# Kernel optimization log

Measured on AMD Instinct MI355X. Metric: run time of the kernel, lower is better.

The kernel has to match this reference:

```python
import jax, jax.numpy as jnp
import numpy as np

B, S, D = 2, 2048, 1024
H, DH = 16, 64  # num_heads, hidden_dimension (per-head)


def setup_inputs() -> dict:
    key = jax.random.key(0)
    ks = jax.random.split(key, 9)
    s = 1.0 / np.sqrt(D)
    so = 1.0 / np.sqrt(H * DH)
    return {
        "x": jax.random.normal(ks[0], (B, S, D), dtype=jnp.float32),
        "Wq": jax.random.uniform(ks[1], (D, H * DH), jnp.float32, -s, s),
        "bq": jax.random.uniform(ks[2], (H * DH,), jnp.float32, -s, s),
        "Wk": jax.random.uniform(ks[3], (D, H * DH), jnp.float32, -s, s),
        "bk": jax.random.uniform(ks[4], (H * DH,), jnp.float32, -s, s),
        "Wv": jax.random.uniform(ks[5], (D, H * DH), jnp.float32, -s, s),
        "bv": jax.random.uniform(ks[6], (H * DH,), jnp.float32, -s, s),
        "Wo": jax.random.uniform(ks[7], (H * DH, D), jnp.float32, -so, so),
        "bo": jax.random.uniform(ks[8], (D,), jnp.float32, -so, so),
    }


def reference(x, Wq, bq, Wk, bk, Wv, bv, Wo, bo):
    b, s, _ = x.shape
    # project and split heads: [b, h, s, dh]
    q = (x @ Wq + bq).reshape(b, s, H, DH).transpose(0, 2, 1, 3)
    k = (x @ Wk + bk).reshape(b, s, H, DH).transpose(0, 2, 1, 3)
    v = (x @ Wv + bv).reshape(b, s, H, DH).transpose(0, 2, 1, 3)
    scores = jnp.einsum('bhqd,bhkd->bhqk', q, k) / jnp.sqrt(jnp.float32(DH))
    causal = jnp.triu(jnp.ones((s, s), dtype=bool), k=1)
    scores = jnp.where(causal, -jnp.inf, scores)
    weights = jax.nn.softmax(scores, axis=-1)
    out = jnp.einsum('bhqk,bhkd->bhqd', weights, v)
    out = out.transpose(0, 2, 1, 3).reshape(b, s, H * DH)
    return out @ Wo + bo
```

## Files before the change

kernel.cpp:

```cpp
#include <hip/hip_runtime.h>

#define B_  2
#define S_  2048
#define D_  1024
#define H_  16
#define DH_ 64
#define NDH (H_*DH_)
#define BS_ (B_*S_)
#define PER ((size_t)B_*H_*S_*DH_)

typedef __bf16 bf16;
typedef bf16 bf16x8 __attribute__((ext_vector_type(8)));
typedef bf16 bf16x4 __attribute__((ext_vector_type(4)));
typedef float f32x4 __attribute__((ext_vector_type(4)));

#define AS1 __attribute__((address_space(1)))
#define AS3 __attribute__((address_space(3)))
__device__ inline void gld16(const bf16* g, bf16* l) {
    __builtin_amdgcn_global_load_lds((const AS1 void*)g, (AS3 void*)l, 16, 0, 0);
}

__global__ __launch_bounds__(256) void prep(
        const float* __restrict__ x,
        const float* __restrict__ W0, const float* __restrict__ W1,
        const float* __restrict__ W2, const float* __restrict__ W3,
        bf16* __restrict__ xb, bf16* __restrict__ T0, bf16* __restrict__ T1,
        bf16* __restrict__ T2, bf16* __restrict__ T3) {
    __shared__ float T[32][33];
    int bid = blockIdx.x, t = threadIdx.x;
    if (bid < 4096) {
        int i = (bid * 256 + t) * 4;
        float4 v = *(const float4*)(x + i);
        bf16x4 o = { (bf16)v.x, (bf16)v.y, (bf16)v.z, (bf16)v.w };
        *(bf16x4*)(xb + i) = o;
        return;
    }
    int r2 = bid - 4096;
    int z = r2 >> 10, w = r2 & 1023;
    const float* W = (z == 0) ? W0 : (z == 1) ? W1 : (z == 2) ? W2 : W3;
    bf16* Wt = (z == 0) ? T0 : (z == 1) ? T1 : (z == 2) ? T2 : T3;
    int k0 = (w >> 5) * 32, n0 = (w & 31) * 32;
    int r = t >> 3, c = (t & 7) * 4;
    float4 v = *(const float4*)(W + (size_t)(k0 + r) * 1024 + n0 + c);
    T[c + 0][r] = v.x; T[c + 1][r] = v.y; T[c + 2][r] = v.z; T[c + 3][r] = v.w;
    __syncthreads();
    bf16x4 o = { (bf16)T[r][c], (bf16)T[r][c + 1], (bf16)T[r][c + 2], (bf16)T[r][c + 3] };
    *(bf16x4*)(Wt + (size_t)(n0 + r) * 1024 + k0 + c) = o;
}

__global__ __launch_bounds__(256) void qkv_gemm(
        const bf16* __restrict__ A, const bf16* __restrict__ Bt,
        const float* __restrict__ bq, const float* __restrict__ bk,
        const float* __restrict__ bv, bf16* __restrict__ Qout, bf16* __restrict__ Vt) {
    __shared__ __align__(16) bf16 As[128 * 32];
    __shared__ __align__(16) bf16 Bs[128 * 32];
    int tid = threadIdx.x, wave = tid >> 6, lane = tid & 63;
    int quad = lane >> 4, l16 = lane & 15;
    int bm = blockIdx.y * 128, bn = blockIdx.x * 128;
    int wm = (wave >> 1) * 64, wn = (wave & 1) * 64;

    int sr = lane >> 2, sc = (lane & 3) * 8;
    const bf16* Ag0 = A + (size_t)(bm + (wave * 2 + 0) * 16 + sr) * 1024 + sc;
    const bf16* Ag1 = A + (size_t)(bm + (wave * 2 + 1) * 16 + sr) * 1024 + sc;
    const bf16* Bg0 = Bt + (size_t)(bn + (wave * 2 + 0) * 16 + sr) * 1024 + sc;
    const bf16* Bg1 = Bt + (size_t)(bn + (wave * 2 + 1) * 16 + sr) * 1024 + sc;
    bf16* Al0 = &As[(wave * 2 + 0) * 512];
    bf16* Al1 = &As[(wave * 2 + 1) * 512];
    bf16* Bl0 = &Bs[(wave * 2 + 0) * 512];
    bf16* Bl1 = &Bs[(wave * 2 + 1) * 512];

    f32x4 acc[4][4] = {};

    for (int k0 = 0; k0 < 1024; k0 += 32) {
        gld16(Ag0 + k0, Al0);
        gld16(Ag1 + k0, Al1);
        gld16(Bg0 + k0, Bl0);
        gld16(Bg1 + k0, Bl1);
        __syncthreads();
        bf16x8 af[4], bfr[4];
        #pragma unroll
        for (int i = 0; i < 4; ++i)
            af[i] = *(const bf16x8*)&As[(wm + i * 16 + l16) * 32 + quad * 8];
        #pragma unroll
        for (int j = 0; j < 4; ++j)
            bfr[j] = *(const bf16x8*)&Bs[(wn + j * 16 + l16) * 32 + quad * 8];
        #pragma unroll
        for (int i = 0; i < 4; ++i)
          #pragma unroll
          for (int j = 0; j < 4; ++j)
            acc[i][j] = __builtin_amdgcn_mfma_f32_16x16x32_bf16(af[i], bfr[j], acc[i][j], 0, 0, 0);
        __syncthreads();
    }

    #pragma unroll
    for (int i = 0; i < 4; ++i)
      #pragma unroll
      for (int j = 0; j < 4; ++j) {
        int col = bn + wn + j * 16 + l16;
        float bias = (col < 1024) ? bq[col] : (col < 2048) ? bk[col - 1024] : bv[col - 2048];
        int qkv = col >> 10, cw = col & 1023;
        int hh = cw >> 6, d = cw & 63;
        int row0 = bm + wm + i * 16 + quad * 4;
        int bb = row0 >> 11, s0 = row0 & 2047;
        if (qkv < 2) {
            #pragma unroll
            for (int r = 0; r < 4; ++r)
                Qout[(size_t)qkv * PER + (((size_t)bb * H_ + hh) * S_ + s0 + r) * DH_ + d] =
                    (bf16)(acc[i][j][r] + bias);
        } else {
            bf16x4 pack;
            #pragma unroll
            for (int r = 0; r < 4; ++r) pack[r] = (bf16)(acc[i][j][r] + bias);
            *(bf16x4*)&Vt[(((size_t)bb * H_ + hh) * DH_ + d) * S_ + s0] = pack;
        }
      }
}

__global__ __launch_bounds__(256) void gemm128f(
        const bf16* __restrict__ A, const bf16* __restrict__ Bt,
        const float* __restrict__ bias, float* __restrict__ out) {
    __shared__ __align__(16) bf16 As[128 * 32];
    __shared__ __align__(16) bf16 Bs[128 * 32];
    int tid = threadIdx.x, wave = tid >> 6, lane = tid & 63;
    int quad = lane >> 4, l16 = lane & 15;
    int bm = blockIdx.y * 128, bn = blockIdx.x * 128;
    int wm = (wave >> 1) * 64, wn = (wave & 1) * 64;

    int sr = lane >> 2, sc = (lane & 3) * 8;
    const bf16* Ag0 = A + (size_t)(bm + (wave * 2 + 0) * 16 + sr) * 1024 + sc;
    const bf16* Ag1 = A + (size_t)(bm + (wave * 2 + 1) * 16 + sr) * 1024 + sc;
    const bf16* Bg0 = Bt + (size_t)(bn + (wave * 2 + 0) * 16 + sr) * 1024 + sc;
    const bf16* Bg1 = Bt + (size_t)(bn + (wave * 2 + 1) * 16 + sr) * 1024 + sc;
    bf16* Al0 = &As[(wave * 2 + 0) * 512];
    bf16* Al1 = &As[(wave * 2 + 1) * 512];
    bf16* Bl0 = &Bs[(wave * 2 + 0) * 512];
    bf16* Bl1 = &Bs[(wave * 2 + 1) * 512];

    f32x4 acc[4][4] = {};

    for (int k0 = 0; k0 < 1024; k0 += 32) {
        gld16(Ag0 + k0, Al0);
        gld16(Ag1 + k0, Al1);
        gld16(Bg0 + k0, Bl0);
        gld16(Bg1 + k0, Bl1);
        __syncthreads();
        bf16x8 af[4], bfr[4];
        #pragma unroll
        for (int i = 0; i < 4; ++i)
            af[i] = *(const bf16x8*)&As[(wm + i * 16 + l16) * 32 + quad * 8];
        #pragma unroll
        for (int j = 0; j < 4; ++j)
            bfr[j] = *(const bf16x8*)&Bs[(wn + j * 16 + l16) * 32 + quad * 8];
        #pragma unroll
        for (int i = 0; i < 4; ++i)
          #pragma unroll
          for (int j = 0; j < 4; ++j)
            acc[i][j] = __builtin_amdgcn_mfma_f32_16x16x32_bf16(af[i], bfr[j], acc[i][j], 0, 0, 0);
        __syncthreads();
    }

    #pragma unroll
    for (int i = 0; i < 4; ++i)
      #pragma unroll
      for (int j = 0; j < 4; ++j) {
        int col = bn + wn + j * 16 + l16;
        float b = bias[col];
        #pragma unroll
        for (int r = 0; r < 4; ++r) {
            int row = bm + wm + i * 16 + quad * 4 + r;
            out[(size_t)row * 1024 + col] = acc[i][j][r] + b;
        }
      }
}

__global__ __launch_bounds__(256) void flash4(
        const bf16* __restrict__ Q, const bf16* __restrict__ K,
        const bf16* __restrict__ Vt, bf16* __restrict__ O) {
    int bh = blockIdx.x;
    int b = bh >> 4, h = bh & 15;
    int pr = blockIdx.y;
    int tid = threadIdx.x;
    int wave = tid >> 6, lane = tid & 63;
    int quad = lane >> 4, l16 = lane & 15;

    __shared__ __align__(16) char smem[4 * 2 * 16 * 72 * 2];
    bf16 (*P)[2][16][72] = reinterpret_cast<bf16 (*)[2][16][72]>(smem);
    float (*redO)[4][64][4] = reinterpret_cast<float (*)[4][64][4]>(smem);
    __shared__ float redL[4][2][4][4];

    const bf16* Qb = Q + (size_t)bh * S_ * DH_;
    const bf16* Kb = K + (size_t)bh * S_ * DH_;
    const bf16* Vb = Vt + (size_t)bh * DH_ * S_;

    bf16x8 ones;
    #pragma unroll
    for (int j = 0; j < 8; ++j) ones[j] = (l16 == 0) ? (bf16)1.0f : (bf16)0.0f;

    for (int half = 0; half < 2; ++half) {
        int tile = half ? (63 - pr) : pr;
        int q0 = tile * 32;

        bf16x8 qf[2][2];
        #pragma unroll
        for (int s = 0; s < 2; ++s) {
            const bf16* qp = Qb + (size_t)(q0 + s * 16 + l16) * DH_ + quad * 8;
            qf[s][0] = *(const bf16x8*)(qp);
            qf[s][1] = *(const bf16x8*)(qp + 32);
        }

        f32x4 oacc[2][4] = {};
        f32x4 lacc[2] = {};

        int nkt = tile / 2 + 1;
        for (int kt = wave; kt < nkt; kt += 4) {
            int kv0 = kt * 64;
            bf16x8 kf[4][2];
            #pragma unroll
            for (int ns = 0; ns < 4; ++ns) {
                const bf16* kp = Kb + (size_t)(kv0 + ns * 16 + l16) * DH_ + quad * 8;
                kf[ns][0] = *(const bf16x8*)(kp);
                kf[ns][1] = *(const bf16x8*)(kp + 32);
            }
            f32x4 sacc[2][4] = {};
            #pragma unroll
            for (int s = 0; s < 2; ++s)
              #pragma unroll
              for (int ns = 0; ns < 4; ++ns) {
                sacc[s][ns] = __builtin_amdgcn_mfma_f32_16x16x32_bf16(qf[s][0], kf[ns][0], sacc[s][ns], 0, 0, 0);
                sacc[s][ns] = __builtin_amdgcn_mfma_f32_16x16x32_bf16(qf[s][1], kf[ns][1], sacc[s][ns], 0, 0, 0);
              }
            bool diag = (kt == nkt - 1);
            #pragma unroll
            for (int s = 0; s < 2; ++s)
              #pragma unroll
              for (int ns = 0; ns < 4; ++ns)
                #pragma unroll
                for (int r = 0; r < 4; ++r) {
                    float p = __expf(sacc[s][ns][r] * 0.125f);
                    if (diag) {
                        int kv = kv0 + ns * 16 + l16;
                        int qq = q0 + s * 16 + quad * 4 + r;
                        if (kv > qq) p = 0.f;
                    }
                    P[wave][s][quad * 4 + r][ns * 16 + l16] = (bf16)p;
                }
            #pragma unroll
            for (int ks = 0; ks < 2; ++ks) {
                bf16x8 pf0 = *(const bf16x8*)&P[wave][0][l16][ks * 32 + quad * 8];
                bf16x8 pf1 = *(const bf16x8*)&P[wave][1][l16][ks * 32 + quad * 8];
                lacc[0] = __builtin_amdgcn_mfma_f32_16x16x32_bf16(pf0, ones, lacc[0], 0, 0, 0);
                lacc[1] = __builtin_amdgcn_mfma_f32_16x16x32_bf16(pf1, ones, lacc[1], 0, 0, 0);
                #pragma unroll
                for (int ds = 0; ds < 4; ++ds) {
                    bf16x8 vf = *(const bf16x8*)(Vb + (size_t)(ds * 16 + l16) * S_ + kv0 + ks * 32 + quad * 8);
                    oacc[0][ds] = __builtin_amdgcn_mfma_f32_16x16x32_bf16(pf0, vf, oacc[0][ds], 0, 0, 0);
                    oacc[1][ds] = __builtin_amdgcn_mfma_f32_16x16x32_bf16(pf1, vf, oacc[1][ds], 0, 0, 0);
                }
            }
        }

        if (l16 == 0) {
            #pragma unroll
            for (int s = 0; s < 2; ++s)
              #pragma unroll
              for (int r = 0; r < 4; ++r)
                redL[wave][s][quad][r] = lacc[s][r];
        }
        #pragma unroll
        for (int s = 0; s < 2; ++s) {
            __syncthreads();
            #pragma unroll
            for (int ds = 0; ds < 4; ++ds)
                *(f32x4*)&redO[wave][ds][lane][0] = oacc[s][ds];
            __syncthreads();
            f32x4 osum = {};
            #pragma unroll
            for (int w = 0; w < 4; ++w)
                osum += *(const f32x4*)&redO[w][wave][lane][0];
            #pragma unroll
            for (int r = 0; r < 4; ++r) {
                float lsum = redL[0][s][quad][r] + redL[1][s][quad][r]
                           + redL[2][s][quad][r] + redL[3][s][quad][r];
                int qq = q0 + s * 16 + quad * 4 + r;
                O[((size_t)b * S_ + qq) * NDH + h * DH_ + wave * 16 + l16] = (bf16)(osum[r] / lsum);
            }
        }
        __syncthreads();
    }
}

extern "C" void kernel_launch(void* const* d_in, const int* in_sizes, int n_in,
                              void* d_out, int out_size, void* d_ws, size_t ws_size,
                              hipStream_t stream) {
    const float* x  = (const float*)d_in[0];
    const float* Wq = (const float*)d_in[1];
    const float* bq = (const float*)d_in[2];
    const float* Wk = (const float*)d_in[3];
    const float* bk = (const float*)d_in[4];
    const float* Wv = (const float*)d_in[5];
    const float* bv = (const float*)d_in[6];
    const float* Wo = (const float*)d_in[7];
    const float* bo = (const float*)d_in[8];
    float* out = (float*)d_out;

    bf16* ws = (bf16*)d_ws;
    const size_t M1 = (size_t)1024 * 1024;
    bf16* xb    = ws;
    bf16* WqkvT = ws + 4 * M1;
    bf16* WoT   = ws + 7 * M1;
    bf16* Qw    = ws + 8 * M1;
    bf16* Vtw   = ws + 16 * M1;
    bf16* Ow    = ws + 20 * M1;

    prep<<<8192, 256, 0, stream>>>(x, Wq, Wk, Wv, Wo,
                                   xb, WqkvT, WqkvT + M1, WqkvT + 2 * M1, WoT);

    qkv_gemm<<<dim3(3072 / 128, BS_ / 128), 256, 0, stream>>>(xb, WqkvT, bq, bk, bv, Qw, Vtw);

    flash4<<<dim3(B_ * H_, 32), 256, 0, stream>>>(Qw, Qw + PER, Vtw, Ow);

    gemm128f<<<dim3(1024 / 128, BS_ / 128), 256, 0, stream>>>(Ow, WoT, bo, out);
}
```

Baseline: 219.5 us.

## Software-pipeline PV step with double-buffered P and fold softmax scale into Q

Folds the 1/sqrt(64)*log2(e) factor into Q at the QKV GEMM epilogue so the attention kernel can use a raw exp2 instead of a scaled __expf. The flash kernel double-buffers the per-wave P tile in shared memory and defers each tile's PV matmul to the next iteration, so it overlaps with the following QK^T and exp work. It also pads P rows to 76 to change LDS bank mapping and adds a launch-bounds occupancy hint. The cost is twice the LDS for P and extra live registers from the pipelining, which could limit occupancy.

```diff
diff --git a/kernel.cpp b/kernel.cpp
--- a/kernel.cpp
+++ b/kernel.cpp
@@ -19,6 +19,14 @@
 __device__ inline void gld16(const bf16* g, bf16* l) {
     __builtin_amdgcn_global_load_lds((const AS1 void*)g, (AS3 void*)l, 16, 0, 0);
 }
+
+#if __has_builtin(__builtin_amdgcn_exp2f)
+#define EXP2(x) __builtin_amdgcn_exp2f(x)
+#else
+#define EXP2(x) exp2f(x)
+#endif
+
+#define QSCALE 0.18033688011112042f
 
 __global__ __launch_bounds__(256) void prep(
         const float* __restrict__ x,
@@ -102,10 +110,15 @@
         int hh = cw >> 6, d = cw & 63;
         int row0 = bm + wm + i * 16 + quad * 4;
         int bb = row0 >> 11, s0 = row0 & 2047;
-        if (qkv < 2) {
+        if (qkv == 0) {
             #pragma unroll
             for (int r = 0; r < 4; ++r)
-                Qout[(size_t)qkv * PER + (((size_t)bb * H_ + hh) * S_ + s0 + r) * DH_ + d] =
+                Qout[(((size_t)bb * H_ + hh) * S_ + s0 + r) * DH_ + d] =
+                    (bf16)((acc[i][j][r] + bias) * QSCALE);
+        } else if (qkv == 1) {
+            #pragma unroll
+            for (int r = 0; r < 4; ++r)
+                Qout[PER + (((size_t)bb * H_ + hh) * S_ + s0 + r) * DH_ + d] =
                     (bf16)(acc[i][j][r] + bias);
         } else {
             bf16x4 pack;
@@ -173,7 +186,8 @@
       }
 }
 
-__global__ __launch_bounds__(256) void flash4(
+#define PPAD 76
+__global__ __launch_bounds__(256, 4) void flash5(
         const bf16* __restrict__ Q, const bf16* __restrict__ K,
         const bf16* __restrict__ Vt, bf16* __restrict__ O) {
     int bh = blockIdx.x;
@@ -183,8 +197,8 @@
     int wave = tid >> 6, lane = tid & 63;
     int quad = lane >> 4, l16 = lane & 15;
 
-    __shared__ __align__(16) char smem[4 * 2 * 16 * 72 * 2];
-    bf16 (*P)[2][16][72] = reinterpret_cast<bf16 (*)[2][16][72]>(smem);
+    __shared__ __align__(16) char smem[2 * 4 * 2 * 16 * PPAD * 2];
+    bf16 (*P)[4][2][16][PPAD] = reinterpret_cast<bf16 (*)[4][2][16][PPAD]>(smem);
     float (*redO)[4][64][4] = reinterpret_cast<float (*)[4][64][4]>(smem);
     __shared__ float redL[4][2][4][4];
 
@@ -211,7 +225,24 @@
         f32x4 oacc[2][4] = {};
         f32x4 lacc[2] = {};
 
+        auto pv_step = [&](int pb, int kv0p) {
+            #pragma unroll
+            for (int ks = 0; ks < 2; ++ks) {
+                bf16x8 pf0 = *(const bf16x8*)&P[pb][wave][0][l16][ks * 32 + quad * 8];
+                bf16x8 pf1 = *(const bf16x8*)&P[pb][wave][1][l16][ks * 32 + quad * 8];
+                lacc[0] = __builtin_amdgcn_mfma_f32_16x16x32_bf16(pf0, ones, lacc[0], 0, 0, 0);
+                lacc[1] = __builtin_amdgcn_mfma_f32_16x16x32_bf16(pf1, ones, lacc[1], 0, 0, 0);
+                #pragma unroll
+                for (int ds = 0; ds < 4; ++ds) {
+                    bf16x8 vf = *(const bf16x8*)(Vb + (size_t)(ds * 16 + l16) * S_ + kv0p + ks * 32 + quad * 8);
+                    oacc[0][ds] = __builtin_amdgcn_mfma_f32_16x16x32_bf16(pf0, vf, oacc[0][ds], 0, 0, 0);
+                    oacc[1][ds] = __builtin_amdgcn_mfma_f32_16x16x32_bf16(pf1, vf, oacc[1][ds], 0, 0, 0);
+                }
+            }
+        };
+
         int nkt = tile / 2 + 1;
+        int buf = 0, kvp = -1;
         for (int kt = wave; kt < nkt; kt += 4) {
             int kv0 = kt * 64;
             bf16x8 kf[4][2];
@@ -221,43 +252,33 @@
                 kf[ns][0] = *(const bf16x8*)(kp);
                 kf[ns][1] = *(const bf16x8*)(kp + 32);
             }
-            f32x4 sacc[2][4] = {};
-            #pragma unroll
-            for (int s = 0; s < 2; ++s)
-              #pragma unroll
-              for (int ns = 0; ns < 4; ++ns) {
-                sacc[s][ns] = __builtin_amdgcn_mfma_f32_16x16x32_bf16(qf[s][0], kf[ns][0], sacc[s][ns], 0, 0, 0);
-                sacc[s][ns] = __builtin_amdgcn_mfma_f32_16x16x32_bf16(qf[s][1], kf[ns][1], sacc[s][ns], 0, 0, 0);
-              }
+            if (kvp >= 0) pv_step(buf ^ 1, kvp);
             bool diag = (kt == nkt - 1);
             #pragma unroll
-            for (int s = 0; s < 2; ++s)
-              #pragma unroll
-              for (int ns = 0; ns < 4; ++ns)
+            for (int s = 0; s < 2; ++s) {
+                f32x4 sacc[4] = {};
                 #pragma unroll
-                for (int r = 0; r < 4; ++r) {
-                    float p = __expf(sacc[s][ns][r] * 0.125f);
+                for (int ns = 0; ns < 4; ++ns) {
+                    sacc[ns] = __builtin_amdgcn_mfma_f32_16x16x32_bf16(qf[s][0], kf[ns][0], sacc[ns], 0, 0, 0);
+                    sacc[ns] = __builtin_amdgcn_mfma_f32_16x16x32_bf16(qf[s][1], kf[ns][1], sacc[ns], 0, 0, 0);
+                }
+                #pragma unroll
+                for (int ns = 0; ns < 4; ++ns)
+                  #pragma unroll
+                  for (int r = 0; r < 4; ++r) {
+                    float p = EXP2(sacc[ns][r]);
                     if (diag) {
                         int kv = kv0 + ns * 16 + l16;
                         int qq = q0 + s * 16 + quad * 4 + r;
                         if (kv > qq) p = 0.f;
                     }
-                    P[wave][s][quad * 4 + r][ns * 16 + l16] = (bf16)p;
-                }
-            #pragma unroll
-            for (int ks = 0; ks < 2; ++ks) {
-                bf16x8 pf0 = *(const bf16x8*)&P[wave][0][l16][ks * 32 + quad * 8];
-                bf16x8 pf1 = *(const bf16x8*)&P[wave][1][l16][ks * 32 + quad * 8];
-                lacc[0] = __builtin_amdgcn_mfma_f32_16x16x32_bf16(pf0, ones, lacc[0], 0, 0, 0);
-                lacc[1] = __builtin_amdgcn_mfma_f32_16x16x32_bf16(pf1, ones, lacc[1], 0, 0, 0);
-                #pragma unroll
-                for (int ds = 0; ds < 4; ++ds) {
-                    bf16x8 vf = *(const bf16x8*)(Vb + (size_t)(ds * 16 + l16) * S_ + kv0 + ks * 32 + quad * 8);
-                    oacc[0][ds] = __builtin_amdgcn_mfma_f32_16x16x32_bf16(pf0, vf, oacc[0][ds], 0, 0, 0);
-                    oacc[1][ds] = __builtin_amdgcn_mfma_f32_16x16x32_bf16(pf1, vf, oacc[1][ds], 0, 0, 0);
-                }
+                    P[buf][wave][s][quad * 4 + r][ns * 16 + l16] = (bf16)p;
+                  }
             }
-        }
+            kvp = kv0;
+            buf ^= 1;
+        }
+        if (kvp >= 0) pv_step(buf ^ 1, kvp);
 
         if (l16 == 0) {
             #pragma unroll
@@ -317,7 +338,7 @@
 
     qkv_gemm<<<dim3(3072 / 128, BS_ / 128), 256, 0, stream>>>(xb, WqkvT, bq, bk, bv, Qw, Vtw);
 
-    flash4<<<dim3(B_ * H_, 32), 256, 0, stream>>>(Qw, Qw + PER, Vtw, Ow);
+    flash5<<<dim3(B_ * H_, 32), 256, 0, stream>>>(Qw, Qw + PER, Vtw, Ow);
 
     gemm128f<<<dim3(1024 / 128, BS_ / 128), 256, 0, stream>>>(Ow, WoT, bo, out);
 }
```

Result: slower. 288.7 us (+31.5%).

## Prefetch next K tile in flash kernel and fold softmax scale into Q

Applied to the files above, without the earlier changes.

The QKV GEMM epilogue now multiplies Q by 0.125*log2(e), so the attention kernel can use exp2 directly on the scores instead of a scale followed by __expf. The flash kernel loads the K fragments for the next tile in two halves, one before and one after the P·V MFMAs, so global loads overlap with compute. P and the reduction buffer now get separate shared-memory arrays, and the P row pitch is padded from 72 to 76 to change the LDS bank pattern. The prefetch raises register pressure and the extra shared memory may lower occupancy; as before, softmax has no max subtraction, and Q is now rounded to bf16 after scaling.

```diff
diff --git a/kernel.cpp b/kernel.cpp
--- a/kernel.cpp
+++ b/kernel.cpp
@@ -19,6 +19,8 @@
 __device__ inline void gld16(const bf16* g, bf16* l) {
     __builtin_amdgcn_global_load_lds((const AS1 void*)g, (AS3 void*)l, 16, 0, 0);
 }
+
+#define QSCALE 0.18033688011112042f
 
 __global__ __launch_bounds__(256) void prep(
         const float* __restrict__ x,
@@ -102,10 +104,15 @@
         int hh = cw >> 6, d = cw & 63;
         int row0 = bm + wm + i * 16 + quad * 4;
         int bb = row0 >> 11, s0 = row0 & 2047;
-        if (qkv < 2) {
+        if (qkv == 0) {
             #pragma unroll
             for (int r = 0; r < 4; ++r)
-                Qout[(size_t)qkv * PER + (((size_t)bb * H_ + hh) * S_ + s0 + r) * DH_ + d] =
+                Qout[(((size_t)bb * H_ + hh) * S_ + s0 + r) * DH_ + d] =
+                    (bf16)((acc[i][j][r] + bias) * QSCALE);
+        } else if (qkv == 1) {
+            #pragma unroll
+            for (int r = 0; r < 4; ++r)
+                Qout[PER + (((size_t)bb * H_ + hh) * S_ + s0 + r) * DH_ + d] =
                     (bf16)(acc[i][j][r] + bias);
         } else {
             bf16x4 pack;
@@ -173,7 +180,8 @@
       }
 }
 
-__global__ __launch_bounds__(256) void flash4(
+#define PPAD 76
+__global__ __launch_bounds__(256) void flash7(
         const bf16* __restrict__ Q, const bf16* __restrict__ K,
         const bf16* __restrict__ Vt, bf16* __restrict__ O) {
     int bh = blockIdx.x;
@@ -183,9 +191,8 @@
     int wave = tid >> 6, lane = tid & 63;
     int quad = lane >> 4, l16 = lane & 15;
 
-    __shared__ __align__(16) char smem[4 * 2 * 16 * 72 * 2];
-    bf16 (*P)[2][16][72] = reinterpret_cast<bf16 (*)[2][16][72]>(smem);
-    float (*redO)[4][64][4] = reinterpret_cast<float (*)[4][64][4]>(smem);
+    __shared__ __align__(16) float redO[4][4][64][4];
+    __shared__ __align__(16) bf16 Pm[4][2][16][PPAD];
     __shared__ float redL[4][2][4][4];
 
     const bf16* Qb = Q + (size_t)bh * S_ * DH_;
@@ -212,23 +219,40 @@
         f32x4 lacc[2] = {};
 
         int nkt = tile / 2 + 1;
+
+        bf16x8 kfa[4][2];
+        {
+            int kt0 = (wave < nkt) ? wave : 0;
+            #pragma unroll
+            for (int ns = 0; ns < 4; ++ns) {
+                const bf16* kp = Kb + (size_t)(kt0 * 64 + ns * 16 + l16) * DH_ + quad * 8;
+                kfa[ns][0] = *(const bf16x8*)(kp);
+                kfa[ns][1] = *(const bf16x8*)(kp + 32);
+            }
+        }
+
         for (int kt = wave; kt < nkt; kt += 4) {
             int kv0 = kt * 64;
-            bf16x8 kf[4][2];
-            #pragma unroll
-            for (int ns = 0; ns < 4; ++ns) {
-                const bf16* kp = Kb + (size_t)(kv0 + ns * 16 + l16) * DH_ + quad * 8;
-                kf[ns][0] = *(const bf16x8*)(kp);
-                kf[ns][1] = *(const bf16x8*)(kp + 32);
-            }
+            int ktn = (kt + 4 < nkt) ? kt + 4 : kt;
+            int kvn = ktn * 64;
+
             f32x4 sacc[2][4] = {};
             #pragma unroll
             for (int s = 0; s < 2; ++s)
               #pragma unroll
               for (int ns = 0; ns < 4; ++ns) {
-                sacc[s][ns] = __builtin_amdgcn_mfma_f32_16x16x32_bf16(qf[s][0], kf[ns][0], sacc[s][ns], 0, 0, 0);
-                sacc[s][ns] = __builtin_amdgcn_mfma_f32_16x16x32_bf16(qf[s][1], kf[ns][1], sacc[s][ns], 0, 0, 0);
+                sacc[s][ns] = __builtin_amdgcn_mfma_f32_16x16x32_bf16(qf[s][0], kfa[ns][0], sacc[s][ns], 0, 0, 0);
+                sacc[s][ns] = __builtin_amdgcn_mfma_f32_16x16x32_bf16(qf[s][1], kfa[ns][1], sacc[s][ns], 0, 0, 0);
               }
+
+            bf16x8 kfb[2][2];
+            #pragma unroll
+            for (int ns = 0; ns < 2; ++ns) {
+                const bf16* kp = Kb + (size_t)(kvn + ns * 16 + l16) * DH_ + quad * 8;
+                kfb[ns][0] = *(const bf16x8*)(kp);
+                kfb[ns][1] = *(const bf16x8*)(kp + 32);
+            }
+
             bool diag = (kt == nkt - 1);
             #pragma unroll
             for (int s = 0; s < 2; ++s)
@@ -236,18 +260,19 @@
               for (int ns = 0; ns < 4; ++ns)
                 #pragma unroll
                 for (int r = 0; r < 4; ++r) {
-                    float p = __expf(sacc[s][ns][r] * 0.125f);
+                    float p = __builtin_exp2f(sacc[s][ns][r]);
                     if (diag) {
                         int kv = kv0 + ns * 16 + l16;
                         int qq = q0 + s * 16 + quad * 4 + r;
                         if (kv > qq) p = 0.f;
                     }
-                    P[wave][s][quad * 4 + r][ns * 16 + l16] = (bf16)p;
+                    Pm[wave][s][quad * 4 + r][ns * 16 + l16] = (bf16)p;
                 }
+
             #pragma unroll
             for (int ks = 0; ks < 2; ++ks) {
-                bf16x8 pf0 = *(const bf16x8*)&P[wave][0][l16][ks * 32 + quad * 8];
-                bf16x8 pf1 = *(const bf16x8*)&P[wave][1][l16][ks * 32 + quad * 8];
+                bf16x8 pf0 = *(const bf16x8*)&Pm[wave][0][l16][ks * 32 + quad * 8];
+                bf16x8 pf1 = *(const bf16x8*)&Pm[wave][1][l16][ks * 32 + quad * 8];
                 lacc[0] = __builtin_amdgcn_mfma_f32_16x16x32_bf16(pf0, ones, lacc[0], 0, 0, 0);
                 lacc[1] = __builtin_amdgcn_mfma_f32_16x16x32_bf16(pf1, ones, lacc[1], 0, 0, 0);
                 #pragma unroll
@@ -256,6 +281,15 @@
                     oacc[0][ds] = __builtin_amdgcn_mfma_f32_16x16x32_bf16(pf0, vf, oacc[0][ds], 0, 0, 0);
                     oacc[1][ds] = __builtin_amdgcn_mfma_f32_16x16x32_bf16(pf1, vf, oacc[1][ds], 0, 0, 0);
                 }
+            }
+
+            kfa[0][0] = kfb[0][0]; kfa[0][1] = kfb[0][1];
+            kfa[1][0] = kfb[1][0]; kfa[1][1] = kfb[1][1];
+            #pragma unroll
+            for (int ns = 2; ns < 4; ++ns) {
+                const bf16* kp = Kb + (size_t)(kvn + ns * 16 + l16) * DH_ + quad * 8;
+                kfa[ns][0] = *(const bf16x8*)(kp);
+                kfa[ns][1] = *(const bf16x8*)(kp + 32);
             }
         }
 
@@ -317,7 +351,7 @@
 
     qkv_gemm<<<dim3(3072 / 128, BS_ / 128), 256, 0, stream>>>(xb, WqkvT, bq, bk, bv, Qw, Vtw);
 
-    flash4<<<dim3(B_ * H_, 32), 256, 0, stream>>>(Qw, Qw + PER, Vtw, Ow);
+    flash7<<<dim3(B_ * H_, 32), 256, 0, stream>>>(Qw, Qw + PER, Vtw, Ow);
 
     gemm128f<<<dim3(1024 / 128, BS_ / 128), 256, 0, stream>>>(Ow, WoT, bo, out);
 }
```

Result: slower. 232.9 us (+6.1%).
